# Optimization experiments

Hardware: AMD Instinct MI355X
Metric: run time of the kernel (lower is better)

The kernel has to match this reference:

```python
import jax, jax.numpy as jnp
import numpy as np

N = 16384      # num_nodes (mamba seq_len)
D = 256        # input_dim
HOPS = 3
E = 262144     # num edges
DI = 512       # d_inner = expand*dim
DS = 16        # d_state
DC = 4         # d_conv


def _ln(x, g, b):
    m = jnp.mean(x, -1, keepdims=True)
    v = jnp.var(x, -1, keepdims=True)
    return (x - m) / jnp.sqrt(v + 1e-5) * g + b


def setup_inputs() -> dict:
    key = jax.random.key(0)
    ks = jax.random.split(key, 20)
    g = lambda i, shape, s=0.02: jax.random.normal(ks[i], shape, jnp.float32) * s
    z = lambda *s: jnp.zeros(s, jnp.float32)
    o = lambda *s: jnp.ones(s, jnp.float32)
    return {
        "x": jax.random.normal(ks[0], (HOPS, N, D), jnp.float32),
        "edge_index": jax.random.randint(ks[1], (2, E), 0, N),
        "perm_noise": jax.random.uniform(ks[2], (N,), jnp.float32),
        "hop_w": g(3, (HOPS * D, D)), "hop_b": z(D), "hop_ln_g": o(D), "hop_ln_b": z(D),
        "gat_w": g(4, (D, D)), "gat_att_src": g(5, (D,)), "gat_att_dst": g(6, (D,)), "gat_b": z(D),
        "in_proj_w": g(7, (D, 2 * DI)),
        "conv_w": g(8, (DI, DC), 0.1),
        "x_proj_w": g(9, (DI, DS + 1)),
        "dt_w": g(10, (1, DI)), "dt_b": z(DI),
        "A_log": g(11, (DI, DS)),
        "D_param": o(DI),
        "out_w": g(12, (DI, D)), "out_b": z(D),
        "mlp_w1": g(13, (2 * D, D)), "mlp_b1": z(D), "mlp_ln_g": o(D), "mlp_ln_b": z(D),
        "mlp_w2": g(14, (D, D)), "mlp_b2": z(D),
    }


def _forward(x, edge_index, perm_noise, hop_w, hop_b, hop_ln_g, hop_ln_b,
             gat_w, gat_att_src, gat_att_dst, gat_b, in_proj_w, conv_w,
             x_proj_w, dt_w, dt_b, A_log, D_param, out_w, out_b,
             mlp_w1, mlp_b1, mlp_ln_g, mlp_ln_b, mlp_w2, mlp_b2):
    n = x.shape[1]
    # [hops,N,D] -> [N, hops*D] -> hop_proj
    xf = jnp.transpose(x, (1, 0, 2)).reshape(n, -1)
    xf = jax.nn.silu(_ln(xf @ hop_w + hop_b, hop_ln_g, hop_ln_b))

    # --- GATConv (heads=1, add_self_loops, negative_slope=0.2, eval dropout) ---
    h = xf @ gat_w                                   # [N,D]
    sl = jnp.arange(n)
    src = jnp.concatenate([edge_index[0], sl])
    dst = jnp.concatenate([edge_index[1], sl])
    e = jax.nn.leaky_relu((h @ gat_att_src)[src] + (h @ gat_att_dst)[dst], 0.2)
    emax = jax.ops.segment_max(e, dst, num_segments=n)
    ee = jnp.exp(e - emax[dst])
    denom = jax.ops.segment_sum(ee, dst, num_segments=n)
    alpha = ee / denom[dst]
    x_mpnn = jax.ops.segment_sum(alpha[:, None] * h[src], dst, num_segments=n) + gat_b

    # --- NodeProcessor: degree-based sort with small random noise ---
    deg = jax.ops.segment_sum(jnp.ones((edge_index.shape[1],), jnp.float32),
                              edge_index[0], num_segments=n)
    sorted_idx = jnp.argsort(deg + perm_noise * 0.1)
    u0 = xf[sorted_idx][None]                        # [1,N,D]

    # --- MambaBlock ---
    xz = u0 @ in_proj_w                              # [1,N,2*DI]
    xm, zgate = jnp.split(xz, 2, axis=-1)
    # depthwise causal conv1d (pad d_conv-1 left == torch pad both + slice[:L])
    xm_t = jnp.transpose(xm, (0, 2, 1))              # [1,DI,N]
    xm_t = jax.lax.conv_general_dilated(xm_t, conv_w[:, None, :], (1,),
                                        [(DC - 1, 0)], feature_group_count=DI)
    xm = jax.nn.silu(jnp.transpose(xm_t, (0, 2, 1)))  # [1,N,DI]
    x_dbl = xm @ x_proj_w                            # [1,N,DS+1]
    dt = jax.nn.softplus(x_dbl[..., :1] @ dt_w + dt_b)  # [1,N,DI]
    Bm = x_dbl[..., 1:]                              # [1,N,DS]
    A = -jnp.exp(A_log)                              # [DI,DS]

    def step(hst, inp):
        dti, Bi = inp                                # [1,DI],[1,DS]
        hst = jnp.exp(A * dti[..., None]) * hst + dti[..., None] * Bi[:, None, :]
        return hst, jnp.einsum('bdn,bn->bd', hst, Bi)

    h0 = jnp.zeros((1, DI, DS), xm.dtype)
    _, ys = jax.lax.scan(step, h0, (jnp.transpose(dt, (1, 0, 2)),
                                    jnp.transpose(Bm, (1, 0, 2))))
    y = jnp.transpose(ys, (1, 0, 2)) + xm * D_param  # [1,N,DI]
    y = y * jax.nn.silu(zgate)
    x_mamba = (y @ out_w + out_b)[0]                 # [N,D]

    reverse_idx = jnp.argsort(sorted_idx)
    x_mamba = x_mamba[reverse_idx]

    cat = jnp.concatenate([x_mpnn, x_mamba], axis=-1)
    out = jax.nn.silu(_ln(cat @ mlp_w1 + mlp_b1, mlp_ln_g, mlp_ln_b)) @ mlp_w2 + mlp_b2
    return out  # dim_proj is Identity (input_dim == output_dim)


def reference(x, edge_index, perm_noise, hop_w, hop_b, hop_ln_g, hop_ln_b,
              gat_w, gat_att_src, gat_att_dst, gat_b, in_proj_w, conv_w,
              x_proj_w, dt_w, dt_b, A_log, D_param, out_w, out_b,
              mlp_w1, mlp_b1, mlp_ln_g, mlp_ln_b, mlp_w2, mlp_b2):
    return _forward(x, edge_index, perm_noise, hop_w, hop_b, hop_ln_g, hop_ln_b,
                    gat_w, gat_att_src, gat_att_dst, gat_b, in_proj_w, conv_w,
                    x_proj_w, dt_w, dt_b, A_log, D_param, out_w, out_b,
                    mlp_w1, mlp_b1, mlp_ln_g, mlp_ln_b, mlp_w2, mlp_b2)
```

## Files before the change

kernel.cpp:

```cpp
#include <hip/hip_runtime.h>

#define N_   16384
#define D_   256
#define E_   262144
#define ET_  278528
#define DI_  512
#define CH_  512
#define CL_  32
#define GS_  16
#define NG_  32

typedef __attribute__((ext_vector_type(8))) short short8;
typedef __attribute__((ext_vector_type(4))) float f32x4;
typedef unsigned short ushort_t;

static __device__ __forceinline__ float wave_sum(float v){
#pragma unroll
  for (int m = 1; m < 64; m <<= 1) v += __shfl_xor(v, m);
  return v;
}
static __device__ __forceinline__ float wave_max(float v){
#pragma unroll
  for (int m = 1; m < 64; m <<= 1) v = fmaxf(v, __shfl_xor(v, m));
  return v;
}
static __device__ __forceinline__ float silu_f(float x){ return x / (1.f + __expf(-x)); }
static __device__ __forceinline__ float softplus_f(float v){
  return fmaxf(v, 0.f) + __logf(1.f + __expf(-fabsf(v)));
}
static __device__ __forceinline__ float fexp2(float x){ return __builtin_amdgcn_exp2f(x); }
static __device__ __forceinline__ ushort_t f2b(float f){
  unsigned u = __float_as_uint(f);
  return (ushort_t)((u + 0x7fffu + ((u >> 16) & 1u)) >> 16);
}
static __device__ __forceinline__ float b2f(ushort_t u){
  return __uint_as_float(((unsigned)u) << 16);
}
#define GLDS16(gp, lp) __builtin_amdgcn_global_load_lds( \
    (const __attribute__((address_space(1))) unsigned int*)(gp), \
    (__attribute__((address_space(3))) unsigned int*)(lp), 16, 0, 0)

__global__ __launch_bounds__(256) void marker_kernel(float* __restrict__ out){
  out[threadIdx.x] = 1e9f;
}

__global__ __launch_bounds__(256) void permute_kernel(const float* __restrict__ x, ushort_t* __restrict__ xcat){
  int idx = blockIdx.x * 256 + threadIdx.x;
  if (idx >= 3 * N_ * 64) return;
  int d4  = idx & 63;
  int n   = (idx >> 6) & (N_ - 1);
  int hop = idx >> 20;
  float4 v = ((const float4*)x)[((size_t)hop << 20) + ((size_t)n << 6) + d4];
  ushort4 o; o.x = f2b(v.x); o.y = f2b(v.y); o.z = f2b(v.z); o.w = f2b(v.w);
  ((ushort4*)xcat)[(size_t)n * 192 + hop * 64 + d4] = o;
}

__global__ __launch_bounds__(256) void wconv_kernel(const float* __restrict__ W, int K, int N,
                                                    ushort_t* __restrict__ BT){
  __shared__ float t[32][33];
  const int k0 = blockIdx.x * 32, n0 = blockIdx.y * 32;
  const int tr = threadIdx.x & 31, tc = threadIdx.x >> 5;
#pragma unroll
  for (int r = tc; r < 32; r += 8) {
    int k = k0 + r, n = n0 + tr;
    t[r][tr] = (k < K && n < N) ? W[(size_t)k * N + n] : 0.f;
  }
  __syncthreads();
#pragma unroll
  for (int r = tc; r < 32; r += 8) {
    int n = n0 + r, k = k0 + tr;
    BT[(size_t)n * K + k] = f2b(t[tr][r]);
  }
}

__global__ __launch_bounds__(256) void mgemm_kernel(
    const ushort_t* __restrict__ A, int lda,
    const ushort_t* __restrict__ BT, int ldbt, int N,
    void* __restrict__ C, int ldc, int c_off, int c_bf16,
    const float* __restrict__ bias, const int* __restrict__ row_map, int K)
{
  __shared__ __align__(16) ushort_t Al[64 * 32];
  __shared__ __align__(16) ushort_t Bl[64 * 32];
  const int tid = threadIdx.x;
  const int lane = tid & 63;
  const int wid = tid >> 6;
  const int wr = wid >> 1, wc = wid & 1;
  const int m0 = blockIdx.x * 64, n0 = blockIdx.y * 64;
  const int fr = lane & 15, fq = lane >> 4;
  const int srow = tid >> 2, scg = (tid & 3) << 3;
  f32x4 acc[2][2] = {};
  for (int k0 = 0; k0 < K; k0 += 32) {
    __syncthreads();
    GLDS16(&A [(size_t)(m0 + srow) * lda  + k0 + scg], &Al[(size_t)wid * 512]);
    GLDS16(&BT[(size_t)(n0 + srow) * ldbt + k0 + scg], &Bl[(size_t)wid * 512]);
    __syncthreads();
    short8 af[2], bfr[2];
#pragma unroll
    for (int m = 0; m < 2; ++m) af[m]  = *(const short8*)&Al[(wr * 32 + m * 16 + fr) * 32 + fq * 8];
#pragma unroll
    for (int n = 0; n < 2; ++n) bfr[n] = *(const short8*)&Bl[(wc * 32 + n * 16 + fr) * 32 + fq * 8];
#pragma unroll
    for (int n = 0; n < 2; ++n)
#pragma unroll
      for (int m = 0; m < 2; ++m)
        acc[m][n] = __builtin_amdgcn_mfma_f32_16x16x32_bf16(af[m], bfr[n], acc[m][n], 0, 0, 0);
  }
#pragma unroll
  for (int m = 0; m < 2; ++m)
#pragma unroll
    for (int n = 0; n < 2; ++n) {
      int col = n0 + wc * 32 + n * 16 + fr;
      if (col >= N) continue;
      float bv = bias ? bias[col] : 0.f;
#pragma unroll
      for (int j = 0; j < 4; ++j) {
        int row = m0 + wr * 32 + m * 16 + fq * 4 + j;
        int orow = row_map ? row_map[row] : row;
        float v = acc[m][n][j] + bv;
        if (c_bf16) ((ushort_t*)C)[(size_t)orow * ldc + c_off + col] = f2b(v);
        else        ((float*)C)   [(size_t)orow * ldc + c_off + col] = v;
      }
    }
}

__global__ __launch_bounds__(256) void ln_silu_kernel(const float* __restrict__ x, ushort_t* __restrict__ o8,
                                                      const float* __restrict__ g, const float* __restrict__ b){
  __shared__ float red[4];
  const int row = blockIdx.x; const int t = threadIdx.x;
  float v = x[(size_t)row * 256 + t];
  float sv = wave_sum(v);
  if ((t & 63) == 0) red[t >> 6] = sv;
  __syncthreads();
  float mean = (red[0] + red[1] + red[2] + red[3]) * (1.f / 256.f);
  __syncthreads();
  float dv = v - mean;
  float sq = wave_sum(dv * dv);
  if ((t & 63) == 0) red[t >> 6] = sq;
  __syncthreads();
  float var = (red[0] + red[1] + red[2] + red[3]) * (1.f / 256.f);
  float o = dv * rsqrtf(var + 1e-5f) * g[t] + b[t];
  o8[(size_t)row * 256 + t] = f2b(silu_f(o));
}

__global__ __launch_bounds__(256) void att_scores_kernel(const ushort_t* __restrict__ h, const float* __restrict__ asr,
                                                         const float* __restrict__ adt, float* __restrict__ as_, float* __restrict__ ad_){
  int wid = threadIdx.x >> 6, lane = threadIdx.x & 63;
  int n = blockIdx.x * 4 + wid;
  float s1 = 0.f, s2 = 0.f;
  for (int f = lane; f < 256; f += 64) {
    float hv = b2f(h[(size_t)n * 256 + f]);
    s1 = fmaf(hv, asr[f], s1); s2 = fmaf(hv, adt[f], s2);
  }
  s1 = wave_sum(s1); s2 = wave_sum(s2);
  if (lane == 0) { as_[n] = s1; ad_[n] = s2; }
}

__global__ __launch_bounds__(256) void count_kernel(const int* __restrict__ ei, int* __restrict__ cnt_in, int* __restrict__ deg_out){
  int i = blockIdx.x * 256 + threadIdx.x;
  if (i >= ET_) return;
  int dst = (i < E_) ? ei[E_ + i] : (i - E_);
  atomicAdd(&cnt_in[dst], 1);
  if (i < E_) atomicAdd(&deg_out[ei[i]], 1);
}

__global__ __launch_bounds__(1024) void scan_offsets_kernel(const int* __restrict__ cnt, int* __restrict__ off, int* __restrict__ cursor){
  __shared__ int part[1024];
  int t = threadIdx.x;
  int base = t * 16;
  int local[16]; int s = 0;
#pragma unroll
  for (int i = 0; i < 16; ++i) { local[i] = s; s += cnt[base + i]; }
  part[t] = s; __syncthreads();
  for (int d = 1; d < 1024; d <<= 1) {
    int val = part[t];
    int add = (t >= d) ? part[t - d] : 0;
    __syncthreads();
    part[t] = val + add;
    __syncthreads();
  }
  int prev = (t > 0) ? part[t - 1] : 0;
#pragma unroll
  for (int i = 0; i < 16; ++i) { int o = prev + local[i]; off[base + i] = o; cursor[base + i] = o; }
  if (t == 1023) off[N_] = part[1023];
}

__global__ __launch_bounds__(256) void scatter_kernel(const int* __restrict__ ei, int* __restrict__ cursor, int* __restrict__ csr){
  int i = blockIdx.x * 256 + threadIdx.x;
  if (i >= ET_) return;
  int dst = (i < E_) ? ei[E_ + i] : (i - E_);
  int pos = atomicAdd(&cursor[dst], 1);
  csr[pos] = i;
}

__global__ __launch_bounds__(256) void gat_agg_kernel(const int* __restrict__ ei, const int* __restrict__ off, const int* __restrict__ csr,
                                                      const float* __restrict__ as_, const float* __restrict__ ad_,
                                                      const ushort_t* __restrict__ h, const float* __restrict__ gat_b, ushort_t* __restrict__ cat){
  const int dst = blockIdx.x;
  const int t = threadIdx.x;
  const int o0 = off[dst];
  int deg = off[dst + 1] - o0;
  if (deg > 1024) deg = 1024;
  __shared__ int   ssrc[1024];
  __shared__ float se[1024];
  __shared__ float red[4];
  const float adv = ad_[dst];
  float m = -1e30f;
  for (int j = t; j < deg; j += 256) {
    int eid = csr[o0 + j];
    int src = (eid < E_) ? ei[eid] : (eid - E_);
    float e = as_[src] + adv;
    e = (e >= 0.f) ? e : 0.2f * e;
    ssrc[j] = src; se[j] = e;
    m = fmaxf(m, e);
  }
  m = wave_max(m);
  if ((t & 63) == 0) red[t >> 6] = m;
  __syncthreads();
  m = fmaxf(fmaxf(red[0], red[1]), fmaxf(red[2], red[3]));
  __syncthreads();
  float dsum = 0.f;
  for (int j = t; j < deg; j += 256) { float x = __expf(se[j] - m); se[j] = x; dsum += x; }
  dsum = wave_sum(dsum);
  if ((t & 63) == 0) red[t >> 6] = dsum;
  __syncthreads();
  float inv = 1.f / (red[0] + red[1] + red[2] + red[3]);
  float acc = gat_b[t];
  for (int j = 0; j < deg; ++j) acc = fmaf(se[j] * inv, b2f(h[(size_t)ssrc[j] * 256 + t]), acc);
  cat[(size_t)dst * 512 + t] = f2b(acc);
}

__global__ __launch_bounds__(256) void key_kernel(const int* __restrict__ degO, const float* __restrict__ noise, unsigned long long* __restrict__ keys){
  int n = blockIdx.x * 256 + threadIdx.x;
  if (n >= N_) return;
  float k = __fadd_rn((float)degO[n], __fmul_rn(noise[n], 0.1f));
  unsigned u = __float_as_uint(k);
  u = (u & 0x80000000u) ? ~u : (u | 0x80000000u);
  keys[n] = ((unsigned long long)u << 32) | (unsigned)n;
}

__global__ __launch_bounds__(256) void rank_part_kernel(const unsigned long long* __restrict__ keys, int* __restrict__ rank){
  __shared__ unsigned long long tile[512];
  const int i = blockIdx.x * 256 + threadIdx.x;
  const unsigned long long ki = keys[i];
  const int base = blockIdx.y * 512;
  for (int j = threadIdx.x; j < 512; j += 256) tile[j] = keys[base + j];
  __syncthreads();
  int r = 0;
#pragma unroll 16
  for (int j = 0; j < 512; ++j) r += (tile[j] < ki);
  atomicAdd(&rank[i], r);
}
__global__ __launch_bounds__(256) void rank_scatter_kernel(const int* __restrict__ rank, int* __restrict__ sidx){
  int i = blockIdx.x * 256 + threadIdx.x;
  sidx[rank[i]] = i;
}

__global__ __launch_bounds__(64) void gather_kernel(const ushort_t* __restrict__ xf, const int* __restrict__ sidx, ushort_t* __restrict__ u0){
  int i = blockIdx.x, t = threadIdx.x;
  ((uint2*)u0)[(size_t)i * 64 + t] = ((const uint2*)xf)[(size_t)sidx[i] * 64 + t];
}

__global__ __launch_bounds__(256) void conv_silu_kernel(const ushort_t* __restrict__ xz, const float* __restrict__ cw, ushort_t* __restrict__ xm){
  int idx = blockIdx.x * 256 + threadIdx.x;
  if (idx >= N_ * 64) return;
  int n = idx >> 6, oc = (idx & 63) << 3;
  float4 cwv[8];
#pragma unroll
  for (int j = 0; j < 8; ++j) cwv[j] = *(const float4*)&cw[(oc + j) * 4];
  short8 tap[4];
#pragma unroll
  for (int k = 0; k < 4; ++k) {
    int nn = n - 3 + k;
    if (nn >= 0) tap[k] = *(const short8*)&xz[(size_t)nn * 1024 + oc];
    else { short8 z = {}; tap[k] = z; }
  }
  float acc[8] = {};
#pragma unroll
  for (int k = 0; k < 4; ++k) {
#pragma unroll
    for (int j = 0; j < 8; ++j) {
      float xv = b2f((ushort_t)tap[k][j]);
      float wv = (&cwv[j].x)[k];
      acc[j] = fmaf(xv, wv, acc[j]);
    }
  }
  short8 o;
#pragma unroll
  for (int j = 0; j < 8; ++j) o[j] = (short)f2b(silu_f(acc[j]));
  *(short8*)&xm[(size_t)n * 512 + oc] = o;
}

__global__ __launch_bounds__(256) void scan_p1_kernel(const float* __restrict__ xdbl,
    const float* __restrict__ dt_w, const float* __restrict__ dt_b, const float* __restrict__ A_log,
    float* __restrict__ a_sum, float* __restrict__ b_final)
{
  const int t = threadIdx.x;
  const int d = blockIdx.x * 256 + t;
  const int c = blockIdx.y;
  float Ac2[16];
#pragma unroll
  for (int k = 0; k < 16; ++k) Ac2[k] = -__expf(A_log[d * 16 + k]) * 1.44269504f;
  const float dwv = dt_w[d], dbv = dt_b[d];
  __shared__ float sx[CL_];
  __shared__ __align__(16) float sB[CL_][16];
  for (int idx = t; idx < CL_ * 17; idx += 256) {
    float v = xdbl[(size_t)c * (CL_ * 17) + idx];
    int row = idx / 17, col = idx - row * 17;
    if (col == 0) sx[row] = v; else sB[row][col - 1] = v;
  }
  __syncthreads();
  float h[16] = {};
  float dts = 0.f;
  for (int i = 0; i < CL_; ++i) {
    float dtv = softplus_f(fmaf(sx[i], dwv, dbv));
    dts += dtv;
    float4 b0 = *(const float4*)&sB[i][0];
    float4 b1 = *(const float4*)&sB[i][4];
    float4 b2 = *(const float4*)&sB[i][8];
    float4 b3 = *(const float4*)&sB[i][12];
    h[0]  = fmaf(fexp2(Ac2[0]  * dtv), h[0],  dtv * b0.x);
    h[1]  = fmaf(fexp2(Ac2[1]  * dtv), h[1],  dtv * b0.y);
    h[2]  = fmaf(fexp2(Ac2[2]  * dtv), h[2],  dtv * b0.z);
    h[3]  = fmaf(fexp2(Ac2[3]  * dtv), h[3],  dtv * b0.w);
    h[4]  = fmaf(fexp2(Ac2[4]  * dtv), h[4],  dtv * b1.x);
    h[5]  = fmaf(fexp2(Ac2[5]  * dtv), h[5],  dtv * b1.y);
    h[6]  = fmaf(fexp2(Ac2[6]  * dtv), h[6],  dtv * b1.z);
    h[7]  = fmaf(fexp2(Ac2[7]  * dtv), h[7],  dtv * b1.w);
    h[8]  = fmaf(fexp2(Ac2[8]  * dtv), h[8],  dtv * b2.x);
    h[9]  = fmaf(fexp2(Ac2[9]  * dtv), h[9],  dtv * b2.y);
    h[10] = fmaf(fexp2(Ac2[10] * dtv), h[10], dtv * b2.z);
    h[11] = fmaf(fexp2(Ac2[11] * dtv), h[11], dtv * b2.w);
    h[12] = fmaf(fexp2(Ac2[12] * dtv), h[12], dtv * b3.x);
    h[13] = fmaf(fexp2(Ac2[13] * dtv), h[13], dtv * b3.y);
    h[14] = fmaf(fexp2(Ac2[14] * dtv), h[14], dtv * b3.z);
    h[15] = fmaf(fexp2(Ac2[15] * dtv), h[15], dtv * b3.w);
  }
  a_sum[c * 512 + d] = dts;
#pragma unroll
  for (int k = 0; k < 16; ++k) b_final[((size_t)c * 16 + k) * 512 + d] = h[k];
}

__global__ __launch_bounds__(256) void scan_mid1_kernel(const float* __restrict__ a_sum,
    const float* __restrict__ b_final, const float* __restrict__ A_log,
    float* __restrict__ ga, float* __restrict__ gb)
{
  const int tid = blockIdx.x * 256 + threadIdx.x;
  const int d = tid & 511;
  const int s = (tid >> 9) & 15;
  const int g = tid >> 13;
  const float Ac = -__expf(A_log[d * 16 + s]);
  const int c0 = g * GS_;
  float ag = 0.f, Bg = 0.f;
  float an = a_sum[c0 * 512 + d];
  float bn = b_final[((size_t)c0 * 16 + s) * 512 + d];
#pragma unroll
  for (int k = 0; k < GS_; ++k) {
    float a = an, b = bn;
    if (k + 1 < GS_) {
      an = a_sum[(c0 + k + 1) * 512 + d];
      bn = b_final[((size_t)(c0 + k + 1) * 16 + s) * 512 + d];
    }
    Bg = fmaf(__expf(Ac * a), Bg, b);
    ag += a;
  }
  gb[((size_t)g * 16 + s) * 512 + d] = Bg;
  if (s == 0) ga[g * 512 + d] = ag;
}

__global__ __launch_bounds__(256) void scan_mid2_kernel(const float* __restrict__ ga,
    const float* __restrict__ gb, const float* __restrict__ A_log, float* __restrict__ ginit)
{
  const int tid = blockIdx.x * 256 + threadIdx.x;
  const int d = tid & 511;
  const int s = tid >> 9;
  const float Ac = -__expf(A_log[d * 16 + s]);
  float gar[NG_], gbr[NG_];
#pragma unroll
  for (int g = 0; g < NG_; ++g) {
    gar[g] = ga[g * 512 + d];
    gbr[g] = gb[((size_t)g * 16 + s) * 512 + d];
  }
  float h = 0.f;
#pragma unroll
  for (int g = 0; g < NG_; ++g) {
    ginit[((size_t)g * 16 + s) * 512 + d] = h;
    h = fmaf(__expf(Ac * gar[g]), h, gbr[g]);
  }
}

__global__ __launch_bounds__(256) void scan_mid3_kernel(const float* __restrict__ a_sum,
    const float* __restrict__ b_final, const float* __restrict__ A_log,
    const float* __restrict__ ginit, float* __restrict__ init)
{
  const int tid = blockIdx.x * 256 + threadIdx.x;
  const int d = tid & 511;
  const int s = (tid >> 9) & 15;
  const int g = tid >> 13;
  const float Ac = -__expf(A_log[d * 16 + s]);
  const int c0 = g * GS_;
  float h = ginit[((size_t)g * 16 + s) * 512 + d];
  float an = a_sum[c0 * 512 + d];
  float bn = b_final[((size_t)c0 * 16 + s) * 512 + d];
#pragma unroll
  for (int k = 0; k < GS_; ++k) {
    float a = an, b = bn;
    if (k + 1 < GS_) {
      an = a_sum[(c0 + k + 1) * 512 + d];
      bn = b_final[((size_t)(c0 + k + 1) * 16 + s) * 512 + d];
    }
    init[((size_t)(c0 + k) * 16 + s) * 512 + d] = h;
    h = fmaf(__expf(Ac * a), h, b);
  }
}

__global__ __launch_bounds__(256) void scan_p3_kernel(const float* __restrict__ xdbl,
    const float* __restrict__ dt_w, const float* __restrict__ dt_b, const float* __restrict__ A_log,
    const float* __restrict__ init, const ushort_t* __restrict__ xm, const float* __restrict__ Dp,
    const ushort_t* __restrict__ xz, ushort_t* __restrict__ y_bf)
{
  const int t = threadIdx.x;
  const int d = blockIdx.x * 256 + t;
  const int c = blockIdx.y;
  float Ac2[16];
#pragma unroll
  for (int k = 0; k < 16; ++k) Ac2[k] = -__expf(A_log[d * 16 + k]) * 1.44269504f;
  const float dwv = dt_w[d], dbv = dt_b[d], dpv = Dp[d];
  __shared__ float sx[CL_];
  __shared__ __align__(16) float sB[CL_][16];
  for (int idx = t; idx < CL_ * 17; idx += 256) {
    float v = xdbl[(size_t)c * (CL_ * 17) + idx];
    int row = idx / 17, col = idx - row * 17;
    if (col == 0) sx[row] = v; else sB[row][col - 1] = v;
  }
  __syncthreads();
  float h[16];
#pragma unroll
  for (int k = 0; k < 16; ++k) h[k] = init[((size_t)c * 16 + k) * 512 + d];
  const int n0 = c * CL_;
  const ushort_t* xmp = xm   + (size_t)n0 * 512  + d;
  const ushort_t* zp  = xz   + (size_t)n0 * 1024 + 512 + d;
  ushort_t*       yp  = y_bf + (size_t)n0 * 512  + d;
  for (int i = 0; i < CL_; ++i) {
    float dtv = softplus_f(fmaf(sx[i], dwv, dbv));
    float4 b0 = *(const float4*)&sB[i][0];
    float4 b1 = *(const float4*)&sB[i][4];
    float4 b2 = *(const float4*)&sB[i][8];
    float4 b3 = *(const float4*)&sB[i][12];
    h[0]  = fmaf(fexp2(Ac2[0]  * dtv), h[0],  dtv * b0.x);
    h[1]  = fmaf(fexp2(Ac2[1]  * dtv), h[1],  dtv * b0.y);
    h[2]  = fmaf(fexp2(Ac2[2]  * dtv), h[2],  dtv * b0.z);
    h[3]  = fmaf(fexp2(Ac2[3]  * dtv), h[3],  dtv * b0.w);
    h[4]  = fmaf(fexp2(Ac2[4]  * dtv), h[4],  dtv * b1.x);
    h[5]  = fmaf(fexp2(Ac2[5]  * dtv), h[5],  dtv * b1.y);
    h[6]  = fmaf(fexp2(Ac2[6]  * dtv), h[6],  dtv * b1.z);
    h[7]  = fmaf(fexp2(Ac2[7]  * dtv), h[7],  dtv * b1.w);
    h[8]  = fmaf(fexp2(Ac2[8]  * dtv), h[8],  dtv * b2.x);
    h[9]  = fmaf(fexp2(Ac2[9]  * dtv), h[9],  dtv * b2.y);
    h[10] = fmaf(fexp2(Ac2[10] * dtv), h[10], dtv * b2.z);
    h[11] = fmaf(fexp2(Ac2[11] * dtv), h[11], dtv * b2.w);
    h[12] = fmaf(fexp2(Ac2[12] * dtv), h[12], dtv * b3.x);
    h[13] = fmaf(fexp2(Ac2[13] * dtv), h[13], dtv * b3.y);
    h[14] = fmaf(fexp2(Ac2[14] * dtv), h[14], dtv * b3.z);
    h[15] = fmaf(fexp2(Ac2[15] * dtv), h[15], dtv * b3.w);
    float y = h[0] * b0.x;
    y = fmaf(h[1],  b0.y, y); y = fmaf(h[2],  b0.z, y); y = fmaf(h[3],  b0.w, y);
    y = fmaf(h[4],  b1.x, y); y = fmaf(h[5],  b1.y, y); y = fmaf(h[6],  b1.z, y);
    y = fmaf(h[7],  b1.w, y); y = fmaf(h[8],  b2.x, y); y = fmaf(h[9],  b2.y, y);
    y = fmaf(h[10], b2.z, y); y = fmaf(h[11], b2.w, y); y = fmaf(h[12], b3.x, y);
    y = fmaf(h[13], b3.y, y); y = fmaf(h[14], b3.z, y); y = fmaf(h[15], b3.w, y);
    float yv = fmaf(b2f(*xmp), dpv, y);
    float z = b2f(*zp);
    *yp = f2b(yv * silu_f(z));
    xmp += 512; zp += 1024; yp += 512;
  }
}

extern "C" void kernel_launch(void* const* d_in, const int* in_sizes, int n_in,
                              void* d_out, int out_size, void* d_ws, size_t ws_size,
                              hipStream_t stream)
{
  (void)in_sizes; (void)n_in; (void)out_size;
  const float* x         = (const float*)d_in[0];
  const int*   ei        = (const int*)d_in[1];
  const float* pnoise    = (const float*)d_in[2];
  const float* hop_w     = (const float*)d_in[3];
  const float* hop_b     = (const float*)d_in[4];
  const float* hop_ln_g  = (const float*)d_in[5];
  const float* hop_ln_b  = (const float*)d_in[6];
  const float* gat_w     = (const float*)d_in[7];
  const float* att_src   = (const float*)d_in[8];
  const float* att_dst   = (const float*)d_in[9];
  const float* gat_b     = (const float*)d_in[10];
  const float* in_proj_w = (const float*)d_in[11];
  const float* conv_w    = (const float*)d_in[12];
  const float* x_proj_w  = (const float*)d_in[13];
  const float* dt_w      = (const float*)d_in[14];
  const float* dt_b      = (const float*)d_in[15];
  const float* A_log     = (const float*)d_in[16];
  const float* D_param   = (const float*)d_in[17];
  const float* out_w     = (const float*)d_in[18];
  const float* out_b     = (const float*)d_in[19];
  const float* mlp_w1    = (const float*)d_in[20];
  const float* mlp_b1    = (const float*)d_in[21];
  const float* mlp_ln_g  = (const float*)d_in[22];
  const float* mlp_ln_b  = (const float*)d_in[23];
  const float* mlp_w2    = (const float*)d_in[24];
  const float* mlp_b2    = (const float*)d_in[25];
  float* out = (float*)d_out;

  char* w = (char*)d_ws;
  auto alloc = [&](size_t bytes) -> void* {
    void* p = (void*)w; w += (bytes + 255) & ~(size_t)255; return p;
  };
  ushort_t* xz_bf  = (ushort_t*)alloc((size_t)N_ * 1024 * 2);
  float*    mlp1f  = (float*)alloc((size_t)N_ * 256 * 4);
  ushort_t* xf_bf  = (ushort_t*)alloc((size_t)N_ * 256 * 2);
  ushort_t* h_bf   = (ushort_t*)alloc((size_t)N_ * 256 * 2);
  ushort_t* u0_bf  = (ushort_t*)alloc((size_t)N_ * 256 * 2);
  ushort_t* xm_bf  = (ushort_t*)alloc((size_t)N_ * 512 * 2);
  ushort_t* y_bf   = (ushort_t*)alloc((size_t)N_ * 512 * 2);
  ushort_t* cat_bf = (ushort_t*)alloc((size_t)N_ * 512 * 2);
  ushort_t* m1_bf  = (ushort_t*)alloc((size_t)N_ * 256 * 2);
  float*    xdbl   = (float*)alloc((size_t)N_ * 17 * 4);
  float*    as_    = (float*)alloc((size_t)N_ * 4);
  float*    ad_    = (float*)alloc((size_t)N_ * 4);
  int* cnt    = (int*)alloc((size_t)N_ * 4);
  int* degO   = (int*)alloc((size_t)N_ * 4);
  int* rank   = (int*)alloc((size_t)N_ * 4);
  int* cursor = (int*)alloc((size_t)N_ * 4);
  int* off    = (int*)alloc((size_t)(N_ + 1) * 4);
  int* sidx   = (int*)alloc((size_t)N_ * 4);
  int* csr    = (int*)alloc((size_t)ET_ * 4);
  unsigned long long* keys = (unsigned long long*)alloc((size_t)N_ * 8);
  float* ga    = (float*)alloc((size_t)NG_ * 512 * 4);
  float* gb    = (float*)alloc((size_t)NG_ * 16 * 512 * 4);
  float* ginit = (float*)alloc((size_t)NG_ * 16 * 512 * 4);
  ushort_t* bt_hop = (ushort_t*)alloc((size_t)256 * 768 * 2);
  ushort_t* bt_gat = (ushort_t*)alloc((size_t)256 * 256 * 2);
  ushort_t* bt_inp = (ushort_t*)alloc((size_t)1024 * 256 * 2);
  ushort_t* bt_xp  = (ushort_t*)alloc((size_t)128 * 512 * 2);
  ushort_t* bt_out = (ushort_t*)alloc((size_t)256 * 512 * 2);
  ushort_t* bt_m1  = (ushort_t*)alloc((size_t)256 * 512 * 2);
  ushort_t* bt_m2  = (ushort_t*)alloc((size_t)256 * 256 * 2);
  ushort_t* xcat_bf = xz_bf;
  float*    b_final = mlp1f;
  float*    init    = (float*)xf_bf;
  float*    a_sum   = (float*)csr;
  size_t needed = (size_t)(w - (char*)d_ws);
  if (needed > ws_size) {
    marker_kernel<<<1, 256, 0, stream>>>(out);
    return;
  }

  hipMemsetAsync(cnt, 0, 3 * (size_t)N_ * 4, stream);

  wconv_kernel<<<dim3(24, 8),  256, 0, stream>>>(hop_w,     768, 256,  bt_hop);
  wconv_kernel<<<dim3(8, 8),   256, 0, stream>>>(gat_w,     256, 256,  bt_gat);
  wconv_kernel<<<dim3(8, 32),  256, 0, stream>>>(in_proj_w, 256, 1024, bt_inp);
  wconv_kernel<<<dim3(16, 4),  256, 0, stream>>>(x_proj_w,  512, 17,   bt_xp);
  wconv_kernel<<<dim3(16, 8),  256, 0, stream>>>(out_w,     512, 256,  bt_out);
  wconv_kernel<<<dim3(16, 8),  256, 0, stream>>>(mlp_w1,    512, 256,  bt_m1);
  wconv_kernel<<<dim3(8, 8),   256, 0, stream>>>(mlp_w2,    256, 256,  bt_m2);

  permute_kernel<<<(3 * N_ * 64) / 256, 256, 0, stream>>>(x, xcat_bf);
  mgemm_kernel<<<dim3(256, 4), 256, 0, stream>>>(xcat_bf, 768, bt_hop, 768, 256, mlp1f, 256, 0, 0, hop_b, nullptr, 768);
  ln_silu_kernel<<<N_, 256, 0, stream>>>(mlp1f, xf_bf, hop_ln_g, hop_ln_b);
  mgemm_kernel<<<dim3(256, 4), 256, 0, stream>>>(xf_bf, 256, bt_gat, 256, 256, h_bf, 256, 0, 1, nullptr, nullptr, 256);
  att_scores_kernel<<<N_ / 4, 256, 0, stream>>>(h_bf, att_src, att_dst, as_, ad_);
  count_kernel<<<(ET_ + 255) / 256, 256, 0, stream>>>(ei, cnt, degO);
  scan_offsets_kernel<<<1, 1024, 0, stream>>>(cnt, off, cursor);
  scatter_kernel<<<(ET_ + 255) / 256, 256, 0, stream>>>(ei, cursor, csr);
  gat_agg_kernel<<<N_, 256, 0, stream>>>(ei, off, csr, as_, ad_, h_bf, gat_b, cat_bf);
  key_kernel<<<N_ / 256, 256, 0, stream>>>(degO, pnoise, keys);
  rank_part_kernel<<<dim3(N_ / 256, 32), 256, 0, stream>>>(keys, rank);
  rank_scatter_kernel<<<N_ / 256, 256, 0, stream>>>(rank, sidx);
  gather_kernel<<<N_, 64, 0, stream>>>(xf_bf, sidx, u0_bf);
  mgemm_kernel<<<dim3(256, 16), 256, 0, stream>>>(u0_bf, 256, bt_inp, 256, 1024, xz_bf, 1024, 0, 1, nullptr, nullptr, 256);
  conv_silu_kernel<<<(N_ * 64) / 256, 256, 0, stream>>>(xz_bf, conv_w, xm_bf);
  mgemm_kernel<<<dim3(256, 1), 256, 0, stream>>>(xm_bf, 512, bt_xp, 512, 17, xdbl, 17, 0, 0, nullptr, nullptr, 512);
  scan_p1_kernel<<<dim3(2, CH_), 256, 0, stream>>>(xdbl, dt_w, dt_b, A_log, a_sum, b_final);
  scan_mid1_kernel<<<(NG_ * 16 * 512) / 256, 256, 0, stream>>>(a_sum, b_final, A_log, ga, gb);
  scan_mid2_kernel<<<32, 256, 0, stream>>>(ga, gb, A_log, ginit);
  scan_mid3_kernel<<<(NG_ * 16 * 512) / 256, 256, 0, stream>>>(a_sum, b_final, A_log, ginit, init);
  scan_p3_kernel<<<dim3(2, CH_), 256, 0, stream>>>(xdbl, dt_w, dt_b, A_log, init, xm_bf, D_param, xz_bf, y_bf);
  mgemm_kernel<<<dim3(256, 4), 256, 0, stream>>>(y_bf, 512, bt_out, 512, 256, cat_bf, 512, 256, 1, out_b, sidx, 512);
  mgemm_kernel<<<dim3(256, 4), 256, 0, stream>>>(cat_bf, 512, bt_m1, 512, 256, mlp1f, 256, 0, 0, mlp_b1, nullptr, 512);
  ln_silu_kernel<<<N_, 256, 0, stream>>>(mlp1f, m1_bf, mlp_ln_g, mlp_ln_b);
  mgemm_kernel<<<dim3(256, 4), 256, 0, stream>>>(m1_bf, 256, bt_m2, 256, 256, out, 256, 0, 0, mlp_b2, nullptr, 256);
}
```

Before: 379.6 us.

## Use one wave per node in GAT aggregation and store scan intermediates in bf16

The GAT aggregation kernel now handles four destination nodes per block, one wavefront each. Each lane accumulates four features with vectorized ushort4 loads, and the block-wide syncthreads reductions become pure wave shuffles. A fallback path for nodes with more than 256 edges recomputes the attention scores instead of caching them, which also removes the old 1024-edge truncation. Separately, the chunked-scan intermediates (b_final, gb, ginit, init) are stored as bf16 rather than fp32 to halve their memory traffic, at some cost in scan-state precision, and the A exponent is computed with exp2.

```diff
diff --git a/kernel.cpp b/kernel.cpp
--- a/kernel.cpp
+++ b/kernel.cpp
@@ -9,6 +9,7 @@
 #define CL_  32
 #define GS_  16
 #define NG_  32
+#define L2E_ 1.44269504f
 
 typedef __attribute__((ext_vector_type(8))) short short8;
 typedef __attribute__((ext_vector_type(4))) float f32x4;
@@ -195,38 +196,75 @@
 __global__ __launch_bounds__(256) void gat_agg_kernel(const int* __restrict__ ei, const int* __restrict__ off, const int* __restrict__ csr,
                                                       const float* __restrict__ as_, const float* __restrict__ ad_,
                                                       const ushort_t* __restrict__ h, const float* __restrict__ gat_b, ushort_t* __restrict__ cat){
-  const int dst = blockIdx.x;
-  const int t = threadIdx.x;
+  const int wv = threadIdx.x >> 6;
+  const int lane = threadIdx.x & 63;
+  const int dst = blockIdx.x * 4 + wv;
+  __shared__ int   ssrc[4][256];
+  __shared__ float se[4][256];
   const int o0 = off[dst];
-  int deg = off[dst + 1] - o0;
-  if (deg > 1024) deg = 1024;
-  __shared__ int   ssrc[1024];
-  __shared__ float se[1024];
-  __shared__ float red[4];
+  const int deg = off[dst + 1] - o0;
   const float adv = ad_[dst];
-  float m = -1e30f;
-  for (int j = t; j < deg; j += 256) {
-    int eid = csr[o0 + j];
-    int src = (eid < E_) ? ei[eid] : (eid - E_);
-    float e = as_[src] + adv;
-    e = (e >= 0.f) ? e : 0.2f * e;
-    ssrc[j] = src; se[j] = e;
-    m = fmaxf(m, e);
-  }
-  m = wave_max(m);
-  if ((t & 63) == 0) red[t >> 6] = m;
-  __syncthreads();
-  m = fmaxf(fmaxf(red[0], red[1]), fmaxf(red[2], red[3]));
-  __syncthreads();
-  float dsum = 0.f;
-  for (int j = t; j < deg; j += 256) { float x = __expf(se[j] - m); se[j] = x; dsum += x; }
-  dsum = wave_sum(dsum);
-  if ((t & 63) == 0) red[t >> 6] = dsum;
-  __syncthreads();
-  float inv = 1.f / (red[0] + red[1] + red[2] + red[3]);
-  float acc = gat_b[t];
-  for (int j = 0; j < deg; ++j) acc = fmaf(se[j] * inv, b2f(h[(size_t)ssrc[j] * 256 + t]), acc);
-  cat[(size_t)dst * 512 + t] = f2b(acc);
+  float4 gb4 = *(const float4*)&gat_b[lane * 4];
+  float a0 = gb4.x, a1 = gb4.y, a2 = gb4.z, a3 = gb4.w;
+  if (deg <= 256) {
+    float m = -1e30f;
+    for (int j = lane; j < deg; j += 64) {
+      int eid = csr[o0 + j];
+      int src = (eid < E_) ? ei[eid] : (eid - E_);
+      float e = as_[src] + adv;
+      e = (e >= 0.f) ? e : 0.2f * e;
+      ssrc[wv][j] = src; se[wv][j] = e;
+      m = fmaxf(m, e);
+    }
+    m = wave_max(m);
+    float dsum = 0.f;
+    for (int j = lane; j < deg; j += 64) {
+      float x = __expf(se[wv][j] - m);
+      se[wv][j] = x; dsum += x;
+    }
+    dsum = wave_sum(dsum);
+    float inv = 1.f / dsum;
+    for (int j = 0; j < deg; ++j) {
+      float wgt = se[wv][j] * inv;
+      int src = ssrc[wv][j];
+      ushort4 hv = *(const ushort4*)&h[(size_t)src * 256 + lane * 4];
+      a0 = fmaf(wgt, b2f(hv.x), a0);
+      a1 = fmaf(wgt, b2f(hv.y), a1);
+      a2 = fmaf(wgt, b2f(hv.z), a2);
+      a3 = fmaf(wgt, b2f(hv.w), a3);
+    }
+  } else {
+    float m = -1e30f;
+    for (int j = lane; j < deg; j += 64) {
+      int eid = csr[o0 + j];
+      int src = (eid < E_) ? ei[eid] : (eid - E_);
+      float e = as_[src] + adv; e = (e >= 0.f) ? e : 0.2f * e;
+      m = fmaxf(m, e);
+    }
+    m = wave_max(m);
+    float dsum = 0.f;
+    for (int j = lane; j < deg; j += 64) {
+      int eid = csr[o0 + j];
+      int src = (eid < E_) ? ei[eid] : (eid - E_);
+      float e = as_[src] + adv; e = (e >= 0.f) ? e : 0.2f * e;
+      dsum += __expf(e - m);
+    }
+    dsum = wave_sum(dsum);
+    float inv = 1.f / dsum;
+    for (int j = 0; j < deg; ++j) {
+      int eid = csr[o0 + j];
+      int src = (eid < E_) ? ei[eid] : (eid - E_);
+      float e = as_[src] + adv; e = (e >= 0.f) ? e : 0.2f * e;
+      float wgt = __expf(e - m) * inv;
+      ushort4 hv = *(const ushort4*)&h[(size_t)src * 256 + lane * 4];
+      a0 = fmaf(wgt, b2f(hv.x), a0);
+      a1 = fmaf(wgt, b2f(hv.y), a1);
+      a2 = fmaf(wgt, b2f(hv.z), a2);
+      a3 = fmaf(wgt, b2f(hv.w), a3);
+    }
+  }
+  ushort4 o; o.x = f2b(a0); o.y = f2b(a1); o.z = f2b(a2); o.w = f2b(a3);
+  *(ushort4*)&cat[(size_t)dst * 512 + lane * 4] = o;
 }
 
 __global__ __launch_bounds__(256) void key_kernel(const int* __restrict__ degO, const float* __restrict__ noise, unsigned long long* __restrict__ keys){
@@ -292,14 +330,14 @@
 
 __global__ __launch_bounds__(256) void scan_p1_kernel(const float* __restrict__ xdbl,
     const float* __restrict__ dt_w, const float* __restrict__ dt_b, const float* __restrict__ A_log,
-    float* __restrict__ a_sum, float* __restrict__ b_final)
+    float* __restrict__ a_sum, ushort_t* __restrict__ b_final)
 {
   const int t = threadIdx.x;
   const int d = blockIdx.x * 256 + t;
   const int c = blockIdx.y;
   float Ac2[16];
 #pragma unroll
-  for (int k = 0; k < 16; ++k) Ac2[k] = -__expf(A_log[d * 16 + k]) * 1.44269504f;
+  for (int k = 0; k < 16; ++k) Ac2[k] = -fexp2(A_log[d * 16 + k] * L2E_) * L2E_;
   const float dwv = dt_w[d], dbv = dt_b[d];
   __shared__ float sx[CL_];
   __shared__ __align__(16) float sB[CL_][16];
@@ -337,85 +375,85 @@
   }
   a_sum[c * 512 + d] = dts;
 #pragma unroll
-  for (int k = 0; k < 16; ++k) b_final[((size_t)c * 16 + k) * 512 + d] = h[k];
+  for (int k = 0; k < 16; ++k) b_final[((size_t)c * 16 + k) * 512 + d] = f2b(h[k]);
 }
 
 __global__ __launch_bounds__(256) void scan_mid1_kernel(const float* __restrict__ a_sum,
-    const float* __restrict__ b_final, const float* __restrict__ A_log,
-    float* __restrict__ ga, float* __restrict__ gb)
+    const ushort_t* __restrict__ b_final, const float* __restrict__ A_log,
+    float* __restrict__ ga, ushort_t* __restrict__ gb)
 {
   const int tid = blockIdx.x * 256 + threadIdx.x;
   const int d = tid & 511;
   const int s = (tid >> 9) & 15;
   const int g = tid >> 13;
-  const float Ac = -__expf(A_log[d * 16 + s]);
+  const float Ac2 = -fexp2(A_log[d * 16 + s] * L2E_) * L2E_;
   const int c0 = g * GS_;
   float ag = 0.f, Bg = 0.f;
   float an = a_sum[c0 * 512 + d];
-  float bn = b_final[((size_t)c0 * 16 + s) * 512 + d];
+  float bn = b2f(b_final[((size_t)c0 * 16 + s) * 512 + d]);
 #pragma unroll
   for (int k = 0; k < GS_; ++k) {
     float a = an, b = bn;
     if (k + 1 < GS_) {
       an = a_sum[(c0 + k + 1) * 512 + d];
-      bn = b_final[((size_t)(c0 + k + 1) * 16 + s) * 512 + d];
-    }
-    Bg = fmaf(__expf(Ac * a), Bg, b);
+      bn = b2f(b_final[((size_t)(c0 + k + 1) * 16 + s) * 512 + d]);
+    }
+    Bg = fmaf(fexp2(Ac2 * a), Bg, b);
     ag += a;
   }
-  gb[((size_t)g * 16 + s) * 512 + d] = Bg;
+  gb[((size_t)g * 16 + s) * 512 + d] = f2b(Bg);
   if (s == 0) ga[g * 512 + d] = ag;
 }
 
 __global__ __launch_bounds__(256) void scan_mid2_kernel(const float* __restrict__ ga,
-    const float* __restrict__ gb, const float* __restrict__ A_log, float* __restrict__ ginit)
+    const ushort_t* __restrict__ gb, const float* __restrict__ A_log, ushort_t* __restrict__ ginit)
 {
   const int tid = blockIdx.x * 256 + threadIdx.x;
   const int d = tid & 511;
   const int s = tid >> 9;
-  const float Ac = -__expf(A_log[d * 16 + s]);
+  const float Ac2 = -fexp2(A_log[d * 16 + s] * L2E_) * L2E_;
   float gar[NG_], gbr[NG_];
 #pragma unroll
   for (int g = 0; g < NG_; ++g) {
     gar[g] = ga[g * 512 + d];
-    gbr[g] = gb[((size_t)g * 16 + s) * 512 + d];
+    gbr[g] = b2f(gb[((size_t)g * 16 + s) * 512 + d]);
   }
   float h = 0.f;
 #pragma unroll
   for (int g = 0; g < NG_; ++g) {
-    ginit[((size_t)g * 16 + s) * 512 + d] = h;
-    h = fmaf(__expf(Ac * gar[g]), h, gbr[g]);
+    ginit[((size_t)g * 16 + s) * 512 + d] = f2b(h);
+    h = fmaf(fexp2(Ac2 * gar[g]), h, gbr[g]);
   }
 }
 
 __global__ __launch_bounds__(256) void scan_mid3_kernel(const float* __restrict__ a_sum,
-    const float* __restrict__ b_final, const float* __restrict__ A_log,
-    const float* __restrict__ ginit, float* __restrict__ init)
+    const ushort_t* __restrict__ b_final, const float* __restrict__ A_log,
+    const ushort_t* __restrict__ ginit, ushort_t* __restrict__ init)
 {
   const int tid = blockIdx.x * 256 + threadIdx.x;
   const int d = tid & 511;
   const int s = (tid >> 9) & 15;
   const int g = tid >> 13;
-  const float Ac = -__expf(A_log[d * 16 + s]);
+  const float Ac2 = -fexp2(A_log[d * 16 + s] * L2E_) * L2E_;
   const int c0 = g * GS_;
-  float h = ginit[((size_t)g * 16 + s) * 512 + d];
+  float h = b2f(ginit[((size_t)g * 16 + s) * 512 + d]);
   float an = a_sum[c0 * 512 + d];
-  float bn = b_final[((size_t)c0 * 16 + s) * 512 + d];
+  float bn = b2f(b_final[((size_t)c0 * 16 + s) * 512 + d]);
 #pragma unroll
   for (int k = 0; k < GS_; ++k) {
     float a = an, b = bn;
     if (k + 1 < GS_) {
       an = a_sum[(c0 + k + 1) * 512 + d];
-      bn = b_final[((size_t)(c0 + k + 1) * 16 + s) * 512 + d];
-    }
-    init[((size_t)(c0 + k) * 16 + s) * 512 + d] = h;
-    h = fmaf(__expf(Ac * a), h, b);
+      bn = b2f(b_final[((size_t)(c0 + k + 1) * 16 + s) * 512 + d]);
+    }
+    init[((size_t)(c0 + k) * 16 + s) * 512 + d] = f2b(h);
+    h = fmaf(fexp2(Ac2 * a), h, b);
   }
 }
 
 __global__ __launch_bounds__(256) void scan_p3_kernel(const float* __restrict__ xdbl,
     const float* __restrict__ dt_w, const float* __restrict__ dt_b, const float* __restrict__ A_log,
-    const float* __restrict__ init, const ushort_t* __restrict__ xm, const float* __restrict__ Dp,
+    const ushort_t* __restrict__ init, const ushort_t* __restrict__ xm, const float* __restrict__ Dp,
     const ushort_t* __restrict__ xz, ushort_t* __restrict__ y_bf)
 {
   const int t = threadIdx.x;
@@ -423,7 +461,7 @@
   const int c = blockIdx.y;
   float Ac2[16];
 #pragma unroll
-  for (int k = 0; k < 16; ++k) Ac2[k] = -__expf(A_log[d * 16 + k]) * 1.44269504f;
+  for (int k = 0; k < 16; ++k) Ac2[k] = -fexp2(A_log[d * 16 + k] * L2E_) * L2E_;
   const float dwv = dt_w[d], dbv = dt_b[d], dpv = Dp[d];
   __shared__ float sx[CL_];
   __shared__ __align__(16) float sB[CL_][16];
@@ -435,7 +473,7 @@
   __syncthreads();
   float h[16];
 #pragma unroll
-  for (int k = 0; k < 16; ++k) h[k] = init[((size_t)c * 16 + k) * 512 + d];
+  for (int k = 0; k < 16; ++k) h[k] = b2f(init[((size_t)c * 16 + k) * 512 + d]);
   const int n0 = c * CL_;
   const ushort_t* xmp = xm   + (size_t)n0 * 512  + d;
   const ushort_t* zp  = xz   + (size_t)n0 * 1024 + 512 + d;
@@ -532,9 +570,9 @@
   int* sidx   = (int*)alloc((size_t)N_ * 4);
   int* csr    = (int*)alloc((size_t)ET_ * 4);
   unsigned long long* keys = (unsigned long long*)alloc((size_t)N_ * 8);
-  float* ga    = (float*)alloc((size_t)NG_ * 512 * 4);
-  float* gb    = (float*)alloc((size_t)NG_ * 16 * 512 * 4);
-  float* ginit = (float*)alloc((size_t)NG_ * 16 * 512 * 4);
+  float*    ga    = (float*)alloc((size_t)NG_ * 512 * 4);
+  ushort_t* gb    = (ushort_t*)alloc((size_t)NG_ * 16 * 512 * 2);
+  ushort_t* ginit = (ushort_t*)alloc((size_t)NG_ * 16 * 512 * 2);
   ushort_t* bt_hop = (ushort_t*)alloc((size_t)256 * 768 * 2);
   ushort_t* bt_gat = (ushort_t*)alloc((size_t)256 * 256 * 2);
   ushort_t* bt_inp = (ushort_t*)alloc((size_t)1024 * 256 * 2);
@@ -543,8 +581,8 @@
   ushort_t* bt_m1  = (ushort_t*)alloc((size_t)256 * 512 * 2);
   ushort_t* bt_m2  = (ushort_t*)alloc((size_t)256 * 256 * 2);
   ushort_t* xcat_bf = xz_bf;
-  float*    b_final = mlp1f;
-  float*    init    = (float*)xf_bf;
+  ushort_t* b_final = (ushort_t*)mlp1f;
+  ushort_t* init    = xf_bf;
   float*    a_sum   = (float*)csr;
   size_t needed = (size_t)(w - (char*)d_ws);
   if (needed > ws_size) {
@@ -570,7 +608,7 @@
   count_kernel<<<(ET_ + 255) / 256, 256, 0, stream>>>(ei, cnt, degO);
   scan_offsets_kernel<<<1, 1024, 0, stream>>>(cnt, off, cursor);
   scatter_kernel<<<(ET_ + 255) / 256, 256, 0, stream>>>(ei, cursor, csr);
-  gat_agg_kernel<<<N_, 256, 0, stream>>>(ei, off, csr, as_, ad_, h_bf, gat_b, cat_bf);
+  gat_agg_kernel<<<N_ / 4, 256, 0, stream>>>(ei, off, csr, as_, ad_, h_bf, gat_b, cat_bf);
   key_kernel<<<N_ / 256, 256, 0, stream>>>(degO, pnoise, keys);
   rank_part_kernel<<<dim3(N_ / 256, 32), 256, 0, stream>>>(keys, rank);
   rank_scatter_kernel<<<N_ / 256, 256, 0, stream>>>(rank, sidx);
```

Measured after the change: 357.1 us. 1.06x faster.
